# Optimization experiments

Measured on AMD Instinct MI355X. Metric: run time of the kernel, lower is better.

Reference implementation:

```python
import jax, jax.numpy as jnp
from jax import lax
import numpy as np

B, L, T = 2048, 2048, 8  # batch, seq_len, num_tags


def setup_inputs() -> dict:
    key = jax.random.key(0)
    k_em, k_len, k_tag, k_tr, k_st, k_en = jax.random.split(key, 6)
    emissions = jax.random.normal(k_em, (B, L, T), dtype=jnp.float32)
    # contiguous valid prefixes (pytorch-crf requires mask[:,0] on, contiguous mask)
    lengths = jax.random.randint(k_len, (B,), L // 2, L + 1)
    valid = jnp.arange(L)[None, :] < lengths[:, None]  # (B, L) bool
    raw = jax.random.randint(k_tag, (B, L), 1, T + 1)  # labels 1..T
    tags = jnp.where(valid, raw, 0).astype(jnp.int64)  # 0 = padding
    transitions = jax.random.normal(k_tr, (T, T), dtype=jnp.float32) * 0.1
    start_transitions = jax.random.normal(k_st, (T,), dtype=jnp.float32) * 0.1
    end_transitions = jax.random.normal(k_en, (T,), dtype=jnp.float32) * 0.1
    return {
        "emissions": emissions,
        "transitions": transitions,
        "start_transitions": start_transitions,
        "end_transitions": end_transitions,
        "tags": tags,
    }


def _crf_nll(emissions, transitions, start_transitions, end_transitions, tags):
    mask = tags != 0                      # (B, L) bool
    shifted = jnp.clip(tags - 1, 0)       # map labels 1..T -> states 0..T-1
    maskf = mask.astype(emissions.dtype)

    # ---- numerator: score of the gold path ----
    em_score = jnp.take_along_axis(emissions, shifted[..., None], axis=2)[..., 0]  # (B, L)
    trans_score = transitions[shifted[:, :-1], shifted[:, 1:]]                      # (B, L-1)
    num = start_transitions[shifted[:, 0]] + em_score[:, 0]
    num = num + jnp.sum((trans_score + em_score[:, 1:]) * maskf[:, 1:], axis=1)
    last_idx = jnp.sum(mask, axis=1) - 1                                            # (B,)
    last_tags = jnp.take_along_axis(shifted, last_idx[:, None], axis=1)[:, 0]
    num = num + end_transitions[last_tags]

    # ---- denominator: log partition via forward algorithm (scan over time) ----
    def step(alpha, xs):
        em_t, m_t = xs  # (B, T), (B,)
        # alpha_next[b, j] = logsumexp_i(alpha[b, i] + trans[i, j] + em_t[b, j])
        nxt = jax.nn.logsumexp(alpha[:, :, None] + transitions[None, :, :], axis=1) + em_t
        alpha = jnp.where(m_t[:, None], nxt, alpha)
        return alpha, None

    alpha0 = start_transitions[None, :] + emissions[:, 0]      # (B, T)
    ems = jnp.swapaxes(emissions[:, 1:], 0, 1)                  # (L-1, B, T)
    ms = jnp.swapaxes(mask[:, 1:], 0, 1)                        # (L-1, B)
    alpha, _ = lax.scan(step, alpha0, (ems, ms))
    denom = jax.nn.logsumexp(alpha + end_transitions[None, :], axis=1)  # (B,)

    llh = num - denom
    return -jnp.mean(llh)  # reduction='mean', wrapper negates log-likelihood


def reference(emissions, transitions, start_transitions, end_transitions, tags):
    return _crf_nll(emissions, transitions, start_transitions, end_transitions, tags)
```

## Files before the change

kernel.cpp:

```cpp
#include <hip/hip_runtime.h>
#include <stdint.h>

typedef float  v4f __attribute__((ext_vector_type(4)));
typedef short  v4s __attribute__((ext_vector_type(4)));
typedef int    v4i __attribute__((ext_vector_type(4)));

#define LOG2E 1.44269504088896340736f
#define LN2   0.69314718055994530942f

static __device__ __forceinline__ float fexp2(float x){ return __builtin_amdgcn_exp2f(x); }
static __device__ __forceinline__ float flog2(float x){ return __builtin_amdgcn_logf(x); }

static __device__ __forceinline__ unsigned pkbf(float a, float b){
  unsigned ua = __float_as_uint(a) + 0x8000u;
  unsigned ub = __float_as_uint(b) + 0x8000u;
  return __builtin_amdgcn_perm(ub, ua, 0x07060302u);
}
static __device__ __forceinline__ v4s pack4(const v4f& m){
  union { unsigned u[2]; v4s s; } t;
  t.u[0] = pkbf(m.x, m.y);
  t.u[1] = pkbf(m.z, m.w);
  return t.s;
}

static __device__ __forceinline__ v4f mfma16(v4s a, v4s b, v4f c){
#if __has_builtin(__builtin_amdgcn_mfma_f32_16x16x16bf16_1k)
  return __builtin_amdgcn_mfma_f32_16x16x16bf16_1k(a, b, c, 0, 0, 0);
#else
  v4f r = c;
  asm("s_nop 1\n\tv_mfma_f32_16x16x16_bf16 %0, %1, %2, %0\n\ts_nop 7\n\ts_nop 1"
      : "+v"(r) : "v"(a), "v"(b));
  return r;
#endif
}

static __device__ __forceinline__ float sel4(const v4f& e4, int s){
  float a = (s & 1) ? e4.y : e4.x;
  float c = (s & 1) ? e4.w : e4.z;
  return (s & 2) ? c : a;
}


template<bool MASKED>
__device__ __forceinline__ void chunk_loop(
    const float* __restrict__ emb, const int* __restrict__ tgb, int nkb, int c,
    const float* s_trans, const float* s_end, float* s_slot,
    v4s afrag, int qr, int r0, int cn, bool lastChunk,
    v4f& master, v4s& bfrag, float& lZ, float& num)
{
  v4f eoA, eoB; v4i tA0 = {}, tA1 = {}, tB0 = {}, tB1 = {};
  int tcA = 0, tpA = 0, tcB = 0, tpB = 0;

  auto loadK = [&](int kb, v4f& eo, v4i& t0v, v4i& t1v, int& tc, int& tp){
    const int t0 = kb << 3;
    eo = *(const v4f*)(emb + (size_t)(t0 + cn) * 8u);
    if (MASKED){
      t0v = *(const v4i*)(tgb + t0);
      t1v = *(const v4i*)(tgb + t0 + 4);
    }
    tc = tgb[t0 + cn];
    int ip = t0 + cn - 1;
    if (!MASKED && c == 0 && ip < 0) ip = 0;
    tp = tgb[ip];
  };

  auto procK = [&](int kb, const v4f& eo, const v4i& t0v, const v4i& t1v,
                   int tc, int tp, bool skipFirst){
    v4f ed;
    ed.x = fexp2(eo.x * LOG2E); ed.y = fexp2(eo.y * LOG2E);
    ed.z = fexp2(eo.z * LOG2E); ed.w = fexp2(eo.w * LOG2E);
    float* sl = s_slot + ((kb & 1) << 5);
    *(v4f*)(sl + (cn << 2)) = ed;
    v4f e8[8];
#pragma unroll
    for (int j = 0; j < 8; ++j) e8[j] = *(const v4f*)(sl + (j << 2));

    {
      bool act = MASKED ? (tc != 0) : true;
      const bool sk0 = (!MASKED) && (c == 0) && (kb == 0) && (cn == 0);
      if (sk0) act = false;
      const int s = tc - 1;
      const float ev = sel4(eo, s);
      num += (act && ((s >> 2) == qr)) ? ev : 0.f;
      const float tv = s_trans[(((tp - 1) & 7) << 3) + (s & 7)];
      num += (act && (qr == 0)) ? tv : 0.f;
      if (MASKED){
        if ((tp != 0) && (tc == 0) && (qr == 0)) num += s_end[tp - 1];
      }
    }

#pragma unroll
    for (int j = 0; j < 8; ++j){
      if (skipFirst && j == 0) continue;
      v4f zero = {0.f, 0.f, 0.f, 0.f};
      v4f d = mfma16(afrag, bfrag, zero);
      const v4f e = e8[j];
      if (MASKED){
        const int ct = (j < 4) ? t0v[j] : t1v[j - 4];
        const bool m = (ct != 0);
        master.x = m ? d.x * e.x : master.x;
        master.y = m ? d.y * e.y : master.y;
        master.z = m ? d.z * e.z : master.z;
        master.w = m ? d.w * e.w : master.w;
      } else {
        master.x = d.x * e.x; master.y = d.y * e.y;
        master.z = d.z * e.z; master.w = d.w * e.w;
      }
      bfrag = pack4(master);
    }
  };

  auto renorm = [&](){
    float mx = fmaxf(fmaxf(master.x, master.y), fmaxf(master.z, master.w));
    mx = fmaxf(mx, __shfl_xor(mx, 16, 64));
    const float inv = __builtin_amdgcn_rcpf(mx);
    master.x *= inv; master.y *= inv; master.z *= inv; master.w *= inv;
    lZ += flog2(mx);
    bfrag = pack4(master);
  };

  loadK(0, eoA, tA0, tA1, tcA, tpA);
#pragma unroll 1
  for (int kb = 0; kb < nkb; kb += 2){
    loadK(kb + 1, eoB, tB0, tB1, tcB, tpB);
    procK(kb, eoA, tA0, tA1, tcA, tpA, (!MASKED) && (c == 0) && (kb == 0));
    if (kb + 2 < nkb) loadK(kb + 2, eoA, tA0, tA1, tcA, tpA);
    procK(kb + 1, eoB, tB0, tB1, tcB, tpB, false);
    renorm();
  }

  if (MASKED && lastChunk){
    const int lt = tgb[(nkb << 3) - 1];
    if ((lt != 0) && (qr == 0) && (cn == 0)) num += s_end[lt - 1];
  }
}

__global__ __launch_bounds__(256, 4)
void crf_phase1(const float* __restrict__ em,
                const float* __restrict__ trans,
                const float* __restrict__ endt,
                const int*   __restrict__ tags,
                float* __restrict__ ws,
                int S, int nC)
{
  const int tid  = threadIdx.x;
  const int lane = tid & 63;
  const int n = lane & 15, q = lane >> 4, qr = q & 1, r0 = qr << 2, cn = n & 7;
  const int mm = ((q >> 1) << 1) | (n >> 3);
  const int p  = (blockIdx.x << 4) + ((tid >> 6) << 2) + mm;
  const int c  = p >> 11;
  const int bm = p & 2047;

  __shared__ float s_trans[64];
  __shared__ float s_end[8];
  __shared__ float s_e[32 * 68];
  if (tid < 64) s_trans[tid] = trans[tid];
  if (tid < 8)  s_end[tid]  = endt[tid];
  __syncthreads();

  v4s afrag;
  {
    float av[4];
#pragma unroll
    for (int j = 0; j < 4; ++j){
      const int k = (q << 2) + j;
      float v = 0.f;
      if (n < 8 && k < 8)        v = fexp2(s_trans[k * 8 + n] * LOG2E);
      else if (n >= 8 && k >= 8) v = fexp2(s_trans[(k - 8) * 8 + (n - 8)] * LOG2E);
      av[j] = v;
    }
    union { unsigned u[2]; v4s s; } t;
    t.u[0] = pkbf(av[0], av[1]);
    t.u[1] = pkbf(av[2], av[3]);
    afrag = t.s;
  }

  const float* emb = em   + ((size_t)bm * 2048u + (size_t)c * (unsigned)S) * 8u + (unsigned)r0;
  const int*   tgb = tags + (size_t)bm * 2048u + (size_t)c * (unsigned)S;
  float* s_slot = &s_e[(tid >> 3) * 68];

  v4f master;
  master.x = (r0 + 0 == cn) ? 1.f : 0.f;
  master.y = (r0 + 1 == cn) ? 1.f : 0.f;
  master.z = (r0 + 2 == cn) ? 1.f : 0.f;
  master.w = (r0 + 3 == cn) ? 1.f : 0.f;
  v4s bfrag = pack4(master);
  float num = 0.f, lZ = 0.f;

  const bool maskless = ((c + 1) * S <= 1024);
  const int  nkb = S >> 3;

  if (maskless){
    chunk_loop<false>(emb, tgb, nkb, c, s_trans, s_end, s_slot,
                      afrag, qr, r0, cn, false, master, bfrag, lZ, num);
  } else {
    const bool fz = (tgb[0] == 0);
    if (__ballot(fz) == ~0ull){
      const int pv = tgb[-1];
      if ((pv != 0) && (qr == 0) && (cn == 0)) num = s_end[pv - 1];
    } else {
      chunk_loop<true>(emb, tgb, nkb, c, s_trans, s_end, s_slot,
                       afrag, qr, r0, cn, (c == nC - 1), master, bfrag, lZ, num);
    }
  }

  float2* ws2 = ((float2*)ws) + (size_t)c * 40u * 2048u + (unsigned)bm;
  const int e0 = (cn << 3) + r0;
  float2 v01; v01.x = master.x; v01.y = master.y;
  float2 v23; v23.x = master.z; v23.y = master.w;
  ws2[(size_t)(e0 >> 1) * 2048u]       = v01;
  ws2[(size_t)((e0 >> 1) + 1) * 2048u] = v23;
  if (qr == 0){
    const int ep = (64 + cn) >> 1;
    ((float*)(ws2 + (size_t)ep * 2048u))[cn & 1] = lZ;
  }
  num += __shfl_xor(num, 1, 64);
  num += __shfl_xor(num, 2, 64);
  num += __shfl_xor(num, 4, 64);
  num += __shfl_xor(num, 16, 64);
  if (qr == 0 && cn == 0)
    ((float*)(ws2 + (size_t)36 * 2048u))[0] = num;
}

__global__ __launch_bounds__(64, 1)
void crf_phase2(const float* __restrict__ em,
                const float* __restrict__ strt,
                const float* __restrict__ endt,
                const int*   __restrict__ tags,
                const float* __restrict__ ws,
                float* __restrict__ out,
                int nC)
{
  const int lane = threadIdx.x;
  const int b = (blockIdx.x << 6) + lane;

  const float* em0 = em + (size_t)b * 16384u;
  float al[8];
#pragma unroll
  for (int i = 0; i < 8; ++i) al[i] = strt[i] + em0[i];
  const int tag0 = tags[(size_t)b * 2048u];
  const int s0 = tag0 - 1;
  float num = strt[s0] + em0[s0];

  float mx = al[0];
#pragma unroll
  for (int i = 1; i < 8; ++i) mx = fmaxf(mx, al[i]);
  float a[8];
#pragma unroll
  for (int i = 0; i < 8; ++i) a[i] = fexp2((al[i] - mx) * LOG2E);
  float lZ2 = mx * LOG2E;

  float P0[64], P1[64], ls0[8], ls1[8], nm0, nm1;

  auto loadC = [&](int c, float* P, float* ls, float& nm){
    const float2* base = ((const float2*)ws) + (size_t)c * 40u * 2048u + (unsigned)b;
#pragma unroll
    for (int i2 = 0; i2 < 32; ++i2){
      float2 v = base[(size_t)i2 * 2048u];
      P[2 * i2] = v.x; P[2 * i2 + 1] = v.y;
    }
#pragma unroll
    for (int k = 0; k < 4; ++k){
      float2 v = base[(size_t)(32 + k) * 2048u];
      ls[2 * k] = v.x; ls[2 * k + 1] = v.y;
    }
    nm = base[(size_t)36 * 2048u].x;
  };

  auto fold = [&](const float* P, const float* ls, float nm){
    float lm = ls[0];
#pragma unroll
    for (int i = 1; i < 8; ++i) lm = fmaxf(lm, ls[i]);
    float w[8];
#pragma unroll
    for (int i = 0; i < 8; ++i) w[i] = a[i] * fexp2(ls[i] - lm);
    float acc[8] = {0.f,0.f,0.f,0.f,0.f,0.f,0.f,0.f};
#pragma unroll
    for (int i = 0; i < 8; ++i)
#pragma unroll
      for (int j = 0; j < 8; ++j)
        acc[j] += w[i] * P[i * 8 + j];
    float m2 = acc[0];
#pragma unroll
    for (int j = 1; j < 8; ++j) m2 = fmaxf(m2, acc[j]);
    const float inv = __builtin_amdgcn_rcpf(m2);
#pragma unroll
    for (int j = 0; j < 8; ++j) a[j] = acc[j] * inv;
    lZ2 += lm + flog2(m2);
    num += nm;
  };

  loadC(0, P0, ls0, nm0);
#pragma unroll 1
  for (int c = 0; c < nC; c += 2){
    loadC(c + 1, P1, ls1, nm1);
    fold(P0, ls0, nm0);
    loadC((c + 2 < nC) ? (c + 2) : (c + 1), P0, ls0, nm0);
    fold(P1, ls1, nm1);
  }

  float accf = 0.f;
#pragma unroll
  for (int j = 0; j < 8; ++j) accf += a[j] * fexp2(endt[j] * LOG2E);
  const float denom = (flog2(accf) + lZ2) * LN2;
  float contrib = (denom - num) * (1.0f / 2048.0f);

#pragma unroll
  for (int off = 32; off; off >>= 1) contrib += __shfl_down(contrib, off, 64);
  if (lane == 0) atomicAdd(out, contrib);
}

extern "C" void kernel_launch(void* const* d_in, const int* in_sizes, int n_in,
                              void* d_out, int out_size, void* d_ws, size_t ws_size,
                              hipStream_t stream) {
  const float* em    = (const float*)d_in[0];
  const float* trans = (const float*)d_in[1];
  const float* strt  = (const float*)d_in[2];
  const float* endt  = (const float*)d_in[3];
  const int*   tags  = (const int*)d_in[4];
  float* out = (float*)d_out;

  const size_t per_chunk = (size_t)2048 * 80 * 4;
  int C;
  if      (ws_size >= 32 * per_chunk) C = 32;
  else if (ws_size >= 16 * per_chunk) C = 16;
  else if (ws_size >=  8 * per_chunk) C = 8;
  else                                C = 4;
  const int S = 2048 / C;

  hipMemsetAsync(out, 0, sizeof(float), stream);
  crf_phase1<<<128 * C, 256, 0, stream>>>(em, trans, endt, tags, (float*)d_ws, S, C);
  crf_phase2<<<32, 64, 0, stream>>>(em, strt, endt, tags, (const float*)d_ws, out, C);
}
```

Baseline: 265.0 us.

## Interleave two independent batch chains per wave and hardcode 32 chunks

Each wave in phase 1 now handles two batch rows at once, interleaving their MFMA dependency chains so the serial matrix-product latency of one hides behind the other. The chunk count is fixed at 32 (64 steps per chunk), which drops the workspace-size-based selection and halves the grid. Phase 2 loses its double-buffered chunk prefetch and gets a higher launch-bounds occupancy hint. The cost is more register pressure in phase 1, and the code now assumes the workspace always holds 32 chunks.

```diff
diff --git a/kernel.cpp b/kernel.cpp
--- a/kernel.cpp
+++ b/kernel.cpp
@@ -42,96 +42,120 @@
 
 
 template<bool MASKED>
-__device__ __forceinline__ void chunk_loop(
-    const float* __restrict__ emb, const int* __restrict__ tgb, int nkb, int c,
-    const float* s_trans, const float* s_end, float* s_slot,
+__device__ __forceinline__ void chunk_loop2(
+    const float* __restrict__ embA, const int* __restrict__ tgbA,
+    const float* __restrict__ embB, const int* __restrict__ tgbB,
+    int c, const float* s_trans, const float* s_end,
+    float* slA, float* slB,
     v4s afrag, int qr, int r0, int cn, bool lastChunk,
-    v4f& master, v4s& bfrag, float& lZ, float& num)
+    v4f& mA, v4s& bfA, float& lZA, float& numA,
+    v4f& mB, v4s& bfB, float& lZB, float& numB)
 {
-  v4f eoA, eoB; v4i tA0 = {}, tA1 = {}, tB0 = {}, tB1 = {};
-  int tcA = 0, tpA = 0, tcB = 0, tpB = 0;
-
-  auto loadK = [&](int kb, v4f& eo, v4i& t0v, v4i& t1v, int& tc, int& tp){
+  v4f eoA[2], eoB[2];
+  v4i tA0[2], tA1[2], tB0[2], tB1[2];
+  int tcA[2], tpA[2], tcB[2], tpB[2];
+
+  auto loadK = [&](const float* __restrict__ emb, const int* __restrict__ tgb,
+                   int kb, int par, v4f (&eo)[2], v4i (&g0)[2], v4i (&g1)[2],
+                   int (&tc)[2], int (&tp)[2]){
     const int t0 = kb << 3;
-    eo = *(const v4f*)(emb + (size_t)(t0 + cn) * 8u);
+    eo[par] = *(const v4f*)(emb + (size_t)(t0 + cn) * 8u);
     if (MASKED){
-      t0v = *(const v4i*)(tgb + t0);
-      t1v = *(const v4i*)(tgb + t0 + 4);
-    }
-    tc = tgb[t0 + cn];
+      g0[par] = *(const v4i*)(tgb + t0);
+      g1[par] = *(const v4i*)(tgb + t0 + 4);
+    }
+    tc[par] = tgb[t0 + cn];
     int ip = t0 + cn - 1;
     if (!MASKED && c == 0 && ip < 0) ip = 0;
-    tp = tgb[ip];
+    tp[par] = tgb[ip];
   };
 
-  auto procK = [&](int kb, const v4f& eo, const v4i& t0v, const v4i& t1v,
-                   int tc, int tp, bool skipFirst){
-    v4f ed;
-    ed.x = fexp2(eo.x * LOG2E); ed.y = fexp2(eo.y * LOG2E);
-    ed.z = fexp2(eo.z * LOG2E); ed.w = fexp2(eo.w * LOG2E);
-    float* sl = s_slot + ((kb & 1) << 5);
-    *(v4f*)(sl + (cn << 2)) = ed;
-    v4f e8[8];
-#pragma unroll
-    for (int j = 0; j < 8; ++j) e8[j] = *(const v4f*)(sl + (j << 2));
-
-    {
-      bool act = MASKED ? (tc != 0) : true;
-      const bool sk0 = (!MASKED) && (c == 0) && (kb == 0) && (cn == 0);
-      if (sk0) act = false;
-      const int s = tc - 1;
-      const float ev = sel4(eo, s);
-      num += (act && ((s >> 2) == qr)) ? ev : 0.f;
-      const float tv = s_trans[(((tp - 1) & 7) << 3) + (s & 7)];
-      num += (act && (qr == 0)) ? tv : 0.f;
-      if (MASKED){
-        if ((tp != 0) && (tc == 0) && (qr == 0)) num += s_end[tp - 1];
-      }
-    }
-
-#pragma unroll
-    for (int j = 0; j < 8; ++j){
-      if (skipFirst && j == 0) continue;
-      v4f zero = {0.f, 0.f, 0.f, 0.f};
-      v4f d = mfma16(afrag, bfrag, zero);
-      const v4f e = e8[j];
-      if (MASKED){
-        const int ct = (j < 4) ? t0v[j] : t1v[j - 4];
-        const bool m = (ct != 0);
-        master.x = m ? d.x * e.x : master.x;
-        master.y = m ? d.y * e.y : master.y;
-        master.z = m ? d.z * e.z : master.z;
-        master.w = m ? d.w * e.w : master.w;
-      } else {
-        master.x = d.x * e.x; master.y = d.y * e.y;
-        master.z = d.z * e.z; master.w = d.w * e.w;
-      }
-      bfrag = pack4(master);
-    }
+  auto numer = [&](const v4f& eo, int tc, int tp, bool sk0, float& num){
+    bool act = MASKED ? (tc != 0) : true;
+    if (sk0) act = false;
+    const int s = tc - 1;
+    const float ev = sel4(eo, s);
+    num += (act && ((s >> 2) == qr)) ? ev : 0.f;
+    const float tv = s_trans[(((tp - 1) & 7) << 3) + (s & 7)];
+    num += (act && (qr == 0)) ? tv : 0.f;
+    if (MASKED && (tp != 0) && (tc == 0) && (qr == 0)) num += s_end[tp - 1];
   };
 
-  auto renorm = [&](){
-    float mx = fmaxf(fmaxf(master.x, master.y), fmaxf(master.z, master.w));
+  auto renorm = [&](v4f& m, v4s& bf, float& lZ){
+    float mx = fmaxf(fmaxf(m.x, m.y), fmaxf(m.z, m.w));
     mx = fmaxf(mx, __shfl_xor(mx, 16, 64));
     const float inv = __builtin_amdgcn_rcpf(mx);
-    master.x *= inv; master.y *= inv; master.z *= inv; master.w *= inv;
+    m.x *= inv; m.y *= inv; m.z *= inv; m.w *= inv;
     lZ += flog2(mx);
-    bfrag = pack4(master);
+    bf = pack4(m);
   };
 
-  loadK(0, eoA, tA0, tA1, tcA, tpA);
-#pragma unroll 1
-  for (int kb = 0; kb < nkb; kb += 2){
-    loadK(kb + 1, eoB, tB0, tB1, tcB, tpB);
-    procK(kb, eoA, tA0, tA1, tcA, tpA, (!MASKED) && (c == 0) && (kb == 0));
-    if (kb + 2 < nkb) loadK(kb + 2, eoA, tA0, tA1, tcA, tpA);
-    procK(kb + 1, eoB, tB0, tB1, tcB, tpB, false);
-    renorm();
+  loadK(embA, tgbA, 0, 0, eoA, tA0, tA1, tcA, tpA);
+  loadK(embB, tgbB, 0, 0, eoB, tB0, tB1, tcB, tpB);
+  loadK(embA, tgbA, 1, 1, eoA, tA0, tA1, tcA, tpA);
+  loadK(embB, tgbB, 1, 1, eoB, tB0, tB1, tcB, tpB);
+
+#pragma unroll 2
+  for (int kb = 0; kb < 8; ++kb){
+    const int par = kb & 1;
+    v4f edA, edB;
+    edA.x = fexp2(eoA[par].x * LOG2E); edA.y = fexp2(eoA[par].y * LOG2E);
+    edA.z = fexp2(eoA[par].z * LOG2E); edA.w = fexp2(eoA[par].w * LOG2E);
+    *(v4f*)(slA + (cn << 2)) = edA;
+    edB.x = fexp2(eoB[par].x * LOG2E); edB.y = fexp2(eoB[par].y * LOG2E);
+    edB.z = fexp2(eoB[par].z * LOG2E); edB.w = fexp2(eoB[par].w * LOG2E);
+    *(v4f*)(slB + (cn << 2)) = edB;
+
+    const bool sk0 = (!MASKED) && (c == 0) && (kb == 0);
+    numer(eoA[par], tcA[par], tpA[par], sk0 && (cn == 0), numA);
+    numer(eoB[par], tcB[par], tpB[par], sk0 && (cn == 0), numB);
+
+    v4i ma0, ma1, mb0, mb1;
+    if (MASKED){ ma0 = tA0[par]; ma1 = tA1[par]; mb0 = tB0[par]; mb1 = tB1[par]; }
+
+    if (kb + 2 < 8){
+      loadK(embA, tgbA, kb + 2, par, eoA, tA0, tA1, tcA, tpA);
+      loadK(embB, tgbB, kb + 2, par, eoB, tB0, tB1, tcB, tpB);
+    }
+
+#pragma unroll
+    for (int j = 0; j < 8; ++j){
+      v4f zero = {0.f, 0.f, 0.f, 0.f};
+      v4f dA = mfma16(afrag, bfA, zero);
+      v4f dB = mfma16(afrag, bfB, zero);
+      v4f eA = *(const v4f*)(slA + (j << 2));
+      v4f eB = *(const v4f*)(slB + (j << 2));
+      if (!(sk0 && j == 0)){
+        if (MASKED){
+          const int ctA = (j < 4) ? ma0[j] : ma1[j - 4];
+          const bool vA = (ctA != 0);
+          mA.x = vA ? dA.x * eA.x : mA.x;
+          mA.y = vA ? dA.y * eA.y : mA.y;
+          mA.z = vA ? dA.z * eA.z : mA.z;
+          mA.w = vA ? dA.w * eA.w : mA.w;
+          const int ctB = (j < 4) ? mb0[j] : mb1[j - 4];
+          const bool vB = (ctB != 0);
+          mB.x = vB ? dB.x * eB.x : mB.x;
+          mB.y = vB ? dB.y * eB.y : mB.y;
+          mB.z = vB ? dB.z * eB.z : mB.z;
+          mB.w = vB ? dB.w * eB.w : mB.w;
+        } else {
+          mA.x = dA.x * eA.x; mA.y = dA.y * eA.y; mA.z = dA.z * eA.z; mA.w = dA.w * eA.w;
+          mB.x = dB.x * eB.x; mB.y = dB.y * eB.y; mB.z = dB.z * eB.z; mB.w = dB.w * eB.w;
+        }
+        bfA = pack4(mA);
+        bfB = pack4(mB);
+      }
+    }
+
+    if (par == 1){ renorm(mA, bfA, lZA); renorm(mB, bfB, lZB); }
   }
 
   if (MASKED && lastChunk){
-    const int lt = tgb[(nkb << 3) - 1];
-    if ((lt != 0) && (qr == 0) && (cn == 0)) num += s_end[lt - 1];
+    const int ltA = tgbA[63];
+    if ((ltA != 0) && (qr == 0) && (cn == 0)) numA += s_end[ltA - 1];
+    const int ltB = tgbB[63];
+    if ((ltB != 0) && (qr == 0) && (cn == 0)) numB += s_end[ltB - 1];
   }
 }
 
@@ -140,20 +164,20 @@
                 const float* __restrict__ trans,
                 const float* __restrict__ endt,
                 const int*   __restrict__ tags,
-                float* __restrict__ ws,
-                int S, int nC)
+                float* __restrict__ ws)
 {
   const int tid  = threadIdx.x;
   const int lane = tid & 63;
   const int n = lane & 15, q = lane >> 4, qr = q & 1, r0 = qr << 2, cn = n & 7;
   const int mm = ((q >> 1) << 1) | (n >> 3);
-  const int p  = (blockIdx.x << 4) + ((tid >> 6) << 2) + mm;
-  const int c  = p >> 11;
-  const int bm = p & 2047;
+  const int pbase = (blockIdx.x << 5) + ((tid >> 6) << 3);
+  const int c   = pbase >> 11;
+  const int bmA = (pbase & 2047) + mm;
+  const int bmB = (pbase & 2047) + 4 + mm;
 
   __shared__ float s_trans[64];
   __shared__ float s_end[8];
-  __shared__ float s_e[32 * 68];
+  __shared__ float s_e[32 * 72];
   if (tid < 64) s_trans[tid] = trans[tid];
   if (tid < 8)  s_end[tid]  = endt[tid];
   __syncthreads();
@@ -175,61 +199,68 @@
     afrag = t.s;
   }
 
-  const float* emb = em   + ((size_t)bm * 2048u + (size_t)c * (unsigned)S) * 8u + (unsigned)r0;
-  const int*   tgb = tags + (size_t)bm * 2048u + (size_t)c * (unsigned)S;
-  float* s_slot = &s_e[(tid >> 3) * 68];
-
-  v4f master;
-  master.x = (r0 + 0 == cn) ? 1.f : 0.f;
-  master.y = (r0 + 1 == cn) ? 1.f : 0.f;
-  master.z = (r0 + 2 == cn) ? 1.f : 0.f;
-  master.w = (r0 + 3 == cn) ? 1.f : 0.f;
-  v4s bfrag = pack4(master);
-  float num = 0.f, lZ = 0.f;
-
-  const bool maskless = ((c + 1) * S <= 1024);
-  const int  nkb = S >> 3;
-
-  if (maskless){
-    chunk_loop<false>(emb, tgb, nkb, c, s_trans, s_end, s_slot,
-                      afrag, qr, r0, cn, false, master, bfrag, lZ, num);
+  const float* embA = em   + ((size_t)bmA * 2048u + (size_t)c * 64u) * 8u + (unsigned)r0;
+  const float* embB = em   + ((size_t)bmB * 2048u + (size_t)c * 64u) * 8u + (unsigned)r0;
+  const int*   tgbA = tags + (size_t)bmA * 2048u + (size_t)c * 64u;
+  const int*   tgbB = tags + (size_t)bmB * 2048u + (size_t)c * 64u;
+  float* slA = &s_e[(tid >> 3) * 72];
+  float* slB = slA + 32;
+
+  v4f mA, mB;
+  mA.x = (r0 + 0 == cn) ? 1.f : 0.f;
+  mA.y = (r0 + 1 == cn) ? 1.f : 0.f;
+  mA.z = (r0 + 2 == cn) ? 1.f : 0.f;
+  mA.w = (r0 + 3 == cn) ? 1.f : 0.f;
+  mB = mA;
+  v4s bfA = pack4(mA), bfB = pack4(mB);
+  float numA = 0.f, lZA = 0.f, numB = 0.f, lZB = 0.f;
+
+  if (c <= 15){
+    chunk_loop2<false>(embA, tgbA, embB, tgbB, c, s_trans, s_end, slA, slB,
+                       afrag, qr, r0, cn, false,
+                       mA, bfA, lZA, numA, mB, bfB, lZB, numB);
   } else {
-    const bool fz = (tgb[0] == 0);
-    if (__ballot(fz) == ~0ull){
-      const int pv = tgb[-1];
-      if ((pv != 0) && (qr == 0) && (cn == 0)) num = s_end[pv - 1];
+    const bool fzA = (tgbA[0] == 0), fzB = (tgbB[0] == 0);
+    if (__ballot(fzA && fzB) == ~0ull){
+      const int pvA = tgbA[-1];
+      if ((pvA != 0) && (qr == 0) && (cn == 0)) numA = s_end[pvA - 1];
+      const int pvB = tgbB[-1];
+      if ((pvB != 0) && (qr == 0) && (cn == 0)) numB = s_end[pvB - 1];
     } else {
-      chunk_loop<true>(emb, tgb, nkb, c, s_trans, s_end, s_slot,
-                       afrag, qr, r0, cn, (c == nC - 1), master, bfrag, lZ, num);
-    }
-  }
-
-  float2* ws2 = ((float2*)ws) + (size_t)c * 40u * 2048u + (unsigned)bm;
-  const int e0 = (cn << 3) + r0;
-  float2 v01; v01.x = master.x; v01.y = master.y;
-  float2 v23; v23.x = master.z; v23.y = master.w;
-  ws2[(size_t)(e0 >> 1) * 2048u]       = v01;
-  ws2[(size_t)((e0 >> 1) + 1) * 2048u] = v23;
-  if (qr == 0){
-    const int ep = (64 + cn) >> 1;
-    ((float*)(ws2 + (size_t)ep * 2048u))[cn & 1] = lZ;
-  }
-  num += __shfl_xor(num, 1, 64);
-  num += __shfl_xor(num, 2, 64);
-  num += __shfl_xor(num, 4, 64);
-  num += __shfl_xor(num, 16, 64);
-  if (qr == 0 && cn == 0)
-    ((float*)(ws2 + (size_t)36 * 2048u))[0] = num;
-}
-
-__global__ __launch_bounds__(64, 1)
+      chunk_loop2<true>(embA, tgbA, embB, tgbB, c, s_trans, s_end, slA, slB,
+                        afrag, qr, r0, cn, (c == 31),
+                        mA, bfA, lZA, numA, mB, bfB, lZB, numB);
+    }
+  }
+
+  auto storeC = [&](int bm, const v4f& m, float lZ, float num){
+    float2* ws2 = ((float2*)ws) + (size_t)c * 40u * 2048u + (unsigned)bm;
+    const int e0 = (cn << 3) + r0;
+    float2 v01; v01.x = m.x; v01.y = m.y;
+    float2 v23; v23.x = m.z; v23.y = m.w;
+    ws2[(size_t)(e0 >> 1) * 2048u]       = v01;
+    ws2[(size_t)((e0 >> 1) + 1) * 2048u] = v23;
+    if (qr == 0)
+      ((float*)(ws2 + (size_t)((64 + cn) >> 1) * 2048u))[cn & 1] = lZ;
+    float nt = num;
+    nt += __shfl_xor(nt, 1, 64);
+    nt += __shfl_xor(nt, 2, 64);
+    nt += __shfl_xor(nt, 4, 64);
+    nt += __shfl_xor(nt, 16, 64);
+    if (qr == 0 && cn == 0)
+      ((float*)(ws2 + (size_t)36 * 2048u))[0] = nt;
+  };
+  storeC(bmA, mA, lZA, numA);
+  storeC(bmB, mB, lZB, numB);
+}
+
+__global__ __launch_bounds__(64, 4)
 void crf_phase2(const float* __restrict__ em,
                 const float* __restrict__ strt,
                 const float* __restrict__ endt,
                 const int*   __restrict__ tags,
                 const float* __restrict__ ws,
-                float* __restrict__ out,
-                int nC)
+                float* __restrict__ out)
 {
   const int lane = threadIdx.x;
   const int b = (blockIdx.x << 6) + lane;
@@ -238,8 +269,7 @@
   float al[8];
 #pragma unroll
   for (int i = 0; i < 8; ++i) al[i] = strt[i] + em0[i];
-  const int tag0 = tags[(size_t)b * 2048u];
-  const int s0 = tag0 - 1;
+  const int s0 = tags[(size_t)b * 2048u] - 1;
   float num = strt[s0] + em0[s0];
 
   float mx = al[0];
@@ -250,10 +280,10 @@
   for (int i = 0; i < 8; ++i) a[i] = fexp2((al[i] - mx) * LOG2E);
   float lZ2 = mx * LOG2E;
 
-  float P0[64], P1[64], ls0[8], ls1[8], nm0, nm1;
-
-  auto loadC = [&](int c, float* P, float* ls, float& nm){
-    const float2* base = ((const float2*)ws) + (size_t)c * 40u * 2048u + (unsigned)b;
+#pragma unroll 1
+  for (int cc = 0; cc < 32; ++cc){
+    const float2* base = ((const float2*)ws) + (size_t)cc * 40u * 2048u + (unsigned)b;
+    float P[64], ls[8];
 #pragma unroll
     for (int i2 = 0; i2 < 32; ++i2){
       float2 v = base[(size_t)i2 * 2048u];
@@ -264,10 +294,8 @@
       float2 v = base[(size_t)(32 + k) * 2048u];
       ls[2 * k] = v.x; ls[2 * k + 1] = v.y;
     }
-    nm = base[(size_t)36 * 2048u].x;
-  };
-
-  auto fold = [&](const float* P, const float* ls, float nm){
+    const float nm = base[(size_t)36 * 2048u].x;
+
     float lm = ls[0];
 #pragma unroll
     for (int i = 1; i < 8; ++i) lm = fmaxf(lm, ls[i]);
@@ -288,15 +316,6 @@
     for (int j = 0; j < 8; ++j) a[j] = acc[j] * inv;
     lZ2 += lm + flog2(m2);
     num += nm;
-  };
-
-  loadC(0, P0, ls0, nm0);
-#pragma unroll 1
-  for (int c = 0; c < nC; c += 2){
-    loadC(c + 1, P1, ls1, nm1);
-    fold(P0, ls0, nm0);
-    loadC((c + 2 < nC) ? (c + 2) : (c + 1), P0, ls0, nm0);
-    fold(P1, ls1, nm1);
   }
 
   float accf = 0.f;
@@ -320,15 +339,7 @@
   const int*   tags  = (const int*)d_in[4];
   float* out = (float*)d_out;
 
-  const size_t per_chunk = (size_t)2048 * 80 * 4;
-  int C;
-  if      (ws_size >= 32 * per_chunk) C = 32;
-  else if (ws_size >= 16 * per_chunk) C = 16;
-  else if (ws_size >=  8 * per_chunk) C = 8;
-  else                                C = 4;
-  const int S = 2048 / C;
-
   hipMemsetAsync(out, 0, sizeof(float), stream);
-  crf_phase1<<<128 * C, 256, 0, stream>>>(em, trans, endt, tags, (float*)d_ws, S, C);
-  crf_phase2<<<32, 64, 0, stream>>>(em, strt, endt, tags, (const float*)d_ws, out, C);
-}
+  crf_phase1<<<2048, 256, 0, stream>>>(em, trans, endt, tags, (float*)d_ws);
+  crf_phase2<<<32, 64, 0, stream>>>(em, strt, endt, tags, (const float*)d_ws, out);
+}
```

Result: slower. 310.3 us (+17.1%).

## Hardcode 32 chunks, fully unroll phase-1 loop, parallelize phase-2 fold across lanes

Applied to the files above, without the earlier changes.

Phase 1 is specialized to 32 chunks of 64 steps. Its inner loop is fully unrolled with triple-buffered loads, and the exp/LDS write for the next block is moved ahead of the current MFMA chain to overlap latency. Phase 2 is restructured from one lane per batch holding the 8x8 chunk matrix in registers to eight lanes per batch using shuffles, with 4-deep prefetch. This raises phase-2 parallelism and cuts its register pressure, but it drops the workspace-size fallback and assumes enough workspace for 32 chunks.

```diff
diff --git a/kernel.cpp b/kernel.cpp
--- a/kernel.cpp
+++ b/kernel.cpp
@@ -43,94 +43,96 @@
 
 template<bool MASKED>
 __device__ __forceinline__ void chunk_loop(
-    const float* __restrict__ emb, const int* __restrict__ tgb, int nkb, int c,
+    const float* __restrict__ emb, const int* __restrict__ tgb, int c,
     const float* s_trans, const float* s_end, float* s_slot,
     v4s afrag, int qr, int r0, int cn, bool lastChunk,
     v4f& master, v4s& bfrag, float& lZ, float& num)
 {
-  v4f eoA, eoB; v4i tA0 = {}, tA1 = {}, tB0 = {}, tB1 = {};
-  int tcA = 0, tpA = 0, tcB = 0, tpB = 0;
-
-  auto loadK = [&](int kb, v4f& eo, v4i& t0v, v4i& t1v, int& tc, int& tp){
+  v4f eo[3]; v4i g0[3], g1[3]; int tc[3], tp[3];
+
+  auto loadK = [&](int kb, int buf){
     const int t0 = kb << 3;
-    eo = *(const v4f*)(emb + (size_t)(t0 + cn) * 8u);
+    eo[buf] = *(const v4f*)(emb + (size_t)(t0 + cn) * 8u);
     if (MASKED){
-      t0v = *(const v4i*)(tgb + t0);
-      t1v = *(const v4i*)(tgb + t0 + 4);
-    }
-    tc = tgb[t0 + cn];
+      g0[buf] = *(const v4i*)(tgb + t0);
+      g1[buf] = *(const v4i*)(tgb + t0 + 4);
+    }
+    tc[buf] = tgb[t0 + cn];
     int ip = t0 + cn - 1;
-    if (!MASKED && c == 0 && ip < 0) ip = 0;
-    tp = tgb[ip];
+    if (c == 0 && ip < 0) ip = 0;
+    tp[buf] = tgb[ip];
   };
 
-  auto procK = [&](int kb, const v4f& eo, const v4i& t0v, const v4i& t1v,
-                   int tc, int tp, bool skipFirst){
+  auto expwrite = [&](const v4f& e, int par){
     v4f ed;
-    ed.x = fexp2(eo.x * LOG2E); ed.y = fexp2(eo.y * LOG2E);
-    ed.z = fexp2(eo.z * LOG2E); ed.w = fexp2(eo.w * LOG2E);
-    float* sl = s_slot + ((kb & 1) << 5);
-    *(v4f*)(sl + (cn << 2)) = ed;
+    ed.x = fexp2(e.x * LOG2E); ed.y = fexp2(e.y * LOG2E);
+    ed.z = fexp2(e.z * LOG2E); ed.w = fexp2(e.w * LOG2E);
+    *(v4f*)(s_slot + (par << 5) + (cn << 2)) = ed;
+  };
+
+  loadK(0, 0); loadK(1, 1); loadK(2, 2);
+  expwrite(eo[0], 0);
+
+#pragma unroll
+  for (int kb = 0; kb < 8; ++kb){
+    const int buf = kb % 3;
+
     v4f e8[8];
+    const float* sl = s_slot + ((kb & 1) << 5);
 #pragma unroll
     for (int j = 0; j < 8; ++j) e8[j] = *(const v4f*)(sl + (j << 2));
 
+    if (kb + 1 < 8) expwrite(eo[(kb + 1) % 3], (kb + 1) & 1);
+
+    const bool sk0 = (!MASKED) && (c == 0) && (kb == 0);
     {
-      bool act = MASKED ? (tc != 0) : true;
-      const bool sk0 = (!MASKED) && (c == 0) && (kb == 0) && (cn == 0);
-      if (sk0) act = false;
-      const int s = tc - 1;
-      const float ev = sel4(eo, s);
+      bool act = MASKED ? (tc[buf] != 0) : true;
+      if (sk0 && cn == 0) act = false;
+      const int s = tc[buf] - 1;
+      const float ev = sel4(eo[buf], s);
       num += (act && ((s >> 2) == qr)) ? ev : 0.f;
-      const float tv = s_trans[(((tp - 1) & 7) << 3) + (s & 7)];
+      const float tv = s_trans[(((tp[buf] - 1) & 7) << 3) + (s & 7)];
       num += (act && (qr == 0)) ? tv : 0.f;
-      if (MASKED){
-        if ((tp != 0) && (tc == 0) && (qr == 0)) num += s_end[tp - 1];
-      }
-    }
+      if (MASKED && (tp[buf] != 0) && (tc[buf] == 0) && (qr == 0))
+        num += s_end[tp[buf] - 1];
+    }
+
+    v4i m0, m1;
+    if (MASKED){ m0 = g0[buf]; m1 = g1[buf]; }
+    if (kb + 3 < 8) loadK(kb + 3, buf);
 
 #pragma unroll
     for (int j = 0; j < 8; ++j){
-      if (skipFirst && j == 0) continue;
+      if (sk0 && j == 0) continue;
       v4f zero = {0.f, 0.f, 0.f, 0.f};
       v4f d = mfma16(afrag, bfrag, zero);
       const v4f e = e8[j];
       if (MASKED){
-        const int ct = (j < 4) ? t0v[j] : t1v[j - 4];
-        const bool m = (ct != 0);
-        master.x = m ? d.x * e.x : master.x;
-        master.y = m ? d.y * e.y : master.y;
-        master.z = m ? d.z * e.z : master.z;
-        master.w = m ? d.w * e.w : master.w;
+        const int ct = (j < 4) ? m0[j] : m1[j - 4];
+        const bool v = (ct != 0);
+        master.x = v ? d.x * e.x : master.x;
+        master.y = v ? d.y * e.y : master.y;
+        master.z = v ? d.z * e.z : master.z;
+        master.w = v ? d.w * e.w : master.w;
       } else {
         master.x = d.x * e.x; master.y = d.y * e.y;
         master.z = d.z * e.z; master.w = d.w * e.w;
       }
       bfrag = pack4(master);
     }
-  };
-
-  auto renorm = [&](){
-    float mx = fmaxf(fmaxf(master.x, master.y), fmaxf(master.z, master.w));
-    mx = fmaxf(mx, __shfl_xor(mx, 16, 64));
-    const float inv = __builtin_amdgcn_rcpf(mx);
-    master.x *= inv; master.y *= inv; master.z *= inv; master.w *= inv;
-    lZ += flog2(mx);
-    bfrag = pack4(master);
-  };
-
-  loadK(0, eoA, tA0, tA1, tcA, tpA);
-#pragma unroll 1
-  for (int kb = 0; kb < nkb; kb += 2){
-    loadK(kb + 1, eoB, tB0, tB1, tcB, tpB);
-    procK(kb, eoA, tA0, tA1, tcA, tpA, (!MASKED) && (c == 0) && (kb == 0));
-    if (kb + 2 < nkb) loadK(kb + 2, eoA, tA0, tA1, tcA, tpA);
-    procK(kb + 1, eoB, tB0, tB1, tcB, tpB, false);
-    renorm();
+
+    if (kb & 1){
+      float mx = fmaxf(fmaxf(master.x, master.y), fmaxf(master.z, master.w));
+      mx = fmaxf(mx, __shfl_xor(mx, 16, 64));
+      const float inv = __builtin_amdgcn_rcpf(mx);
+      master.x *= inv; master.y *= inv; master.z *= inv; master.w *= inv;
+      lZ += flog2(mx);
+      bfrag = pack4(master);
+    }
   }
 
   if (MASKED && lastChunk){
-    const int lt = tgb[(nkb << 3) - 1];
+    const int lt = tgb[63];
     if ((lt != 0) && (qr == 0) && (cn == 0)) num += s_end[lt - 1];
   }
 }
@@ -140,8 +142,7 @@
                 const float* __restrict__ trans,
                 const float* __restrict__ endt,
                 const int*   __restrict__ tags,
-                float* __restrict__ ws,
-                int S, int nC)
+                float* __restrict__ ws)
 {
   const int tid  = threadIdx.x;
   const int lane = tid & 63;
@@ -175,8 +176,8 @@
     afrag = t.s;
   }
 
-  const float* emb = em   + ((size_t)bm * 2048u + (size_t)c * (unsigned)S) * 8u + (unsigned)r0;
-  const int*   tgb = tags + (size_t)bm * 2048u + (size_t)c * (unsigned)S;
+  const float* emb = em   + ((size_t)bm * 2048u + (size_t)c * 64u) * 8u + (unsigned)r0;
+  const int*   tgb = tags + (size_t)bm * 2048u + (size_t)c * 64u;
   float* s_slot = &s_e[(tid >> 3) * 68];
 
   v4f master;
@@ -187,11 +188,8 @@
   v4s bfrag = pack4(master);
   float num = 0.f, lZ = 0.f;
 
-  const bool maskless = ((c + 1) * S <= 1024);
-  const int  nkb = S >> 3;
-
-  if (maskless){
-    chunk_loop<false>(emb, tgb, nkb, c, s_trans, s_end, s_slot,
+  if (c <= 15){
+    chunk_loop<false>(emb, tgb, c, s_trans, s_end, s_slot,
                       afrag, qr, r0, cn, false, master, bfrag, lZ, num);
   } else {
     const bool fz = (tgb[0] == 0);
@@ -199,8 +197,8 @@
       const int pv = tgb[-1];
       if ((pv != 0) && (qr == 0) && (cn == 0)) num = s_end[pv - 1];
     } else {
-      chunk_loop<true>(emb, tgb, nkb, c, s_trans, s_end, s_slot,
-                       afrag, qr, r0, cn, (c == nC - 1), master, bfrag, lZ, num);
+      chunk_loop<true>(emb, tgb, c, s_trans, s_end, s_slot,
+                       afrag, qr, r0, cn, (c == 31), master, bfrag, lZ, num);
     }
   }
 
@@ -210,10 +208,8 @@
   float2 v23; v23.x = master.z; v23.y = master.w;
   ws2[(size_t)(e0 >> 1) * 2048u]       = v01;
   ws2[(size_t)((e0 >> 1) + 1) * 2048u] = v23;
-  if (qr == 0){
-    const int ep = (64 + cn) >> 1;
-    ((float*)(ws2 + (size_t)ep * 2048u))[cn & 1] = lZ;
-  }
+  if (qr == 0)
+    ((float*)(ws2 + (size_t)((64 + cn) >> 1) * 2048u))[cn & 1] = lZ;
   num += __shfl_xor(num, 1, 64);
   num += __shfl_xor(num, 2, 64);
   num += __shfl_xor(num, 4, 64);
@@ -222,91 +218,82 @@
     ((float*)(ws2 + (size_t)36 * 2048u))[0] = num;
 }
 
-__global__ __launch_bounds__(64, 1)
+__global__ __launch_bounds__(256, 4)
 void crf_phase2(const float* __restrict__ em,
                 const float* __restrict__ strt,
                 const float* __restrict__ endt,
                 const int*   __restrict__ tags,
                 const float* __restrict__ ws,
-                float* __restrict__ out,
-                int nC)
+                float* __restrict__ out)
 {
-  const int lane = threadIdx.x;
-  const int b = (blockIdx.x << 6) + lane;
-
-  const float* em0 = em + (size_t)b * 16384u;
-  float al[8];
-#pragma unroll
-  for (int i = 0; i < 8; ++i) al[i] = strt[i] + em0[i];
-  const int tag0 = tags[(size_t)b * 2048u];
-  const int s0 = tag0 - 1;
-  float num = strt[s0] + em0[s0];
-
-  float mx = al[0];
-#pragma unroll
-  for (int i = 1; i < 8; ++i) mx = fmaxf(mx, al[i]);
-  float a[8];
-#pragma unroll
-  for (int i = 0; i < 8; ++i) a[i] = fexp2((al[i] - mx) * LOG2E);
+  const int tid  = threadIdx.x;
+  const int lane = tid & 63;
+  const int gt = (blockIdx.x << 8) + tid;
+  const int b = gt >> 3;
+  const int j = gt & 7;
+  const int gbase = lane & 56;
+
+  const unsigned poff = ((unsigned)(j >> 1) << 12) + (unsigned)(j & 1) + ((unsigned)b << 1);
+  const float* wsf = ws;
+
+  const float al = strt[j] + em[(size_t)b * 16384u + (unsigned)j];
+  const int s0 = tags[(size_t)b * 2048u] - 1;
+  float num = __shfl(al, gbase + s0, 64);
+
+  float mx = al;
+  mx = fmaxf(mx, __shfl_xor(mx, 1, 64));
+  mx = fmaxf(mx, __shfl_xor(mx, 2, 64));
+  mx = fmaxf(mx, __shfl_xor(mx, 4, 64));
+  float a = fexp2((al - mx) * LOG2E);
   float lZ2 = mx * LOG2E;
 
-  float P0[64], P1[64], ls0[8], ls1[8], nm0, nm1;
-
-  auto loadC = [&](int c, float* P, float* ls, float& nm){
-    const float2* base = ((const float2*)ws) + (size_t)c * 40u * 2048u + (unsigned)b;
-#pragma unroll
-    for (int i2 = 0; i2 < 32; ++i2){
-      float2 v = base[(size_t)i2 * 2048u];
-      P[2 * i2] = v.x; P[2 * i2 + 1] = v.y;
-    }
-#pragma unroll
-    for (int k = 0; k < 4; ++k){
-      float2 v = base[(size_t)(32 + k) * 2048u];
-      ls[2 * k] = v.x; ls[2 * k + 1] = v.y;
-    }
-    nm = base[(size_t)36 * 2048u].x;
+  float Pb[4][8], lsb[4], nmb[4];
+  auto loadChunk = [&](int c, int s){
+    const float* base = wsf + (size_t)c * 163840u;
+#pragma unroll
+    for (int i = 0; i < 8; ++i) Pb[s][i] = base[poff + (unsigned)i * 16384u];
+    lsb[s] = base[131072u + poff];
+    nmb[s] = base[147456u + ((unsigned)b << 1)];
   };
 
-  auto fold = [&](const float* P, const float* ls, float nm){
-    float lm = ls[0];
-#pragma unroll
-    for (int i = 1; i < 8; ++i) lm = fmaxf(lm, ls[i]);
-    float w[8];
-#pragma unroll
-    for (int i = 0; i < 8; ++i) w[i] = a[i] * fexp2(ls[i] - lm);
-    float acc[8] = {0.f,0.f,0.f,0.f,0.f,0.f,0.f,0.f};
+  loadChunk(0, 0); loadChunk(1, 1); loadChunk(2, 2);
+
+#pragma unroll 4
+  for (int c = 0; c < 32; ++c){
+    const int s = c & 3;
+    if (c + 3 < 32) loadChunk(c + 3, (c + 3) & 3);
+
+    float ls = lsb[s];
+    float lm = ls;
+    lm = fmaxf(lm, __shfl_xor(lm, 1, 64));
+    lm = fmaxf(lm, __shfl_xor(lm, 2, 64));
+    lm = fmaxf(lm, __shfl_xor(lm, 4, 64));
+    const float w = a * fexp2(ls - lm);
+
+    float acc = 0.f;
 #pragma unroll
     for (int i = 0; i < 8; ++i)
-#pragma unroll
-      for (int j = 0; j < 8; ++j)
-        acc[j] += w[i] * P[i * 8 + j];
-    float m2 = acc[0];
-#pragma unroll
-    for (int j = 1; j < 8; ++j) m2 = fmaxf(m2, acc[j]);
-    const float inv = __builtin_amdgcn_rcpf(m2);
-#pragma unroll
-    for (int j = 0; j < 8; ++j) a[j] = acc[j] * inv;
+      acc += __shfl(w, gbase + i, 64) * Pb[s][i];
+
+    float m2 = acc;
+    m2 = fmaxf(m2, __shfl_xor(m2, 1, 64));
+    m2 = fmaxf(m2, __shfl_xor(m2, 2, 64));
+    m2 = fmaxf(m2, __shfl_xor(m2, 4, 64));
+    a = acc * __builtin_amdgcn_rcpf(m2);
     lZ2 += lm + flog2(m2);
-    num += nm;
-  };
-
-  loadC(0, P0, ls0, nm0);
-#pragma unroll 1
-  for (int c = 0; c < nC; c += 2){
-    loadC(c + 1, P1, ls1, nm1);
-    fold(P0, ls0, nm0);
-    loadC((c + 2 < nC) ? (c + 2) : (c + 1), P0, ls0, nm0);
-    fold(P1, ls1, nm1);
-  }
-
-  float accf = 0.f;
-#pragma unroll
-  for (int j = 0; j < 8; ++j) accf += a[j] * fexp2(endt[j] * LOG2E);
-  const float denom = (flog2(accf) + lZ2) * LN2;
-  float contrib = (denom - num) * (1.0f / 2048.0f);
-
-#pragma unroll
-  for (int off = 32; off; off >>= 1) contrib += __shfl_down(contrib, off, 64);
+    num += nmb[s];
+  }
+
+  float t = a * fexp2(endt[j] * LOG2E);
+  t += __shfl_xor(t, 1, 64);
+  t += __shfl_xor(t, 2, 64);
+  t += __shfl_xor(t, 4, 64);
+  const float denom = (flog2(t) + lZ2) * LN2;
+
+  float contrib = (j == 0) ? (denom - num) * (1.0f / 2048.0f) : 0.f;
+  contrib += __shfl_xor(contrib, 8, 64);
+  contrib += __shfl_xor(contrib, 16, 64);
+  contrib += __shfl_xor(contrib, 32, 64);
   if (lane == 0) atomicAdd(out, contrib);
 }
 
@@ -320,15 +307,7 @@
   const int*   tags  = (const int*)d_in[4];
   float* out = (float*)d_out;
 
-  const size_t per_chunk = (size_t)2048 * 80 * 4;
-  int C;
-  if      (ws_size >= 32 * per_chunk) C = 32;
-  else if (ws_size >= 16 * per_chunk) C = 16;
-  else if (ws_size >=  8 * per_chunk) C = 8;
-  else                                C = 4;
-  const int S = 2048 / C;
-
   hipMemsetAsync(out, 0, sizeof(float), stream);
-  crf_phase1<<<128 * C, 256, 0, stream>>>(em, trans, endt, tags, (float*)d_ws, S, C);
-  crf_phase2<<<32, 64, 0, stream>>>(em, strt, endt, tags, (const float*)d_ws, out, C);
-}
+  crf_phase1<<<4096, 256, 0, stream>>>(em, trans, endt, tags, (float*)d_ws);
+  crf_phase2<<<64, 256, 0, stream>>>(em, strt, endt, tags, (const float*)d_ws, out);
+}
```

New measurement: 243.7 us. 8.1% less time.
